# Performance work log

Measured on AMD Instinct MI355X. Metric: run time of the kernel, lower is better.

## Reference

```python
import jax, jax.numpy as jnp
import numpy as np

N_HEAD = 16

def setup_inputs() -> dict:
    key = jax.random.key(0)
    ks = jax.random.split(key, 5)
    d = 1024
    x = jax.random.normal(ks[0], (2, 2048, d), dtype=jnp.float32)
    Wqkv = jax.random.normal(ks[1], (d, 3 * d), dtype=jnp.float32) * (1.0 / np.sqrt(d))
    bqkv = jnp.zeros((3 * d,), dtype=jnp.float32)
    Wproj = jax.random.normal(ks[2], (d, d), dtype=jnp.float32) * (1.0 / np.sqrt(d))
    bproj = jnp.zeros((d,), dtype=jnp.float32)
    return {"x": x, "Wqkv": Wqkv, "bqkv": bqkv, "Wproj": Wproj, "bproj": bproj}


def reference(x, Wqkv, bqkv, Wproj, bproj):
    B, T, C = x.shape
    H = N_HEAD
    Dh = C // H
    qkv = x @ Wqkv + bqkv                      # [B, T, 3C]
    q, k, v = jnp.split(qkv, 3, axis=-1)
    # [B, T, C] -> [B, H, T, Dh]
    q = q.reshape(B, T, H, Dh).transpose(0, 2, 1, 3)
    k = k.reshape(B, T, H, Dh).transpose(0, 2, 1, 3)
    v = v.reshape(B, T, H, Dh).transpose(0, 2, 1, 3)
    scale = 1.0 / np.sqrt(Dh)
    att = jnp.einsum('bhqd,bhkd->bhqk', q, k) * scale
    causal = jnp.tril(jnp.ones((T, T), dtype=bool))
    att = jnp.where(causal[None, None, :, :], att, jnp.float32(-jnp.inf))
    att = jax.nn.softmax(att, axis=-1)
    y = jnp.einsum('bhqk,bhkd->bhqd', att, v)  # [B, H, T, Dh]
    y = y.transpose(0, 2, 1, 3).reshape(B, T, C)
    return y @ Wproj + bproj
```

## Files before the change

kernel.cpp:

```cpp
#include <hip/hip_runtime.h>
#include <math.h>


typedef __attribute__((ext_vector_type(8))) short short8;
typedef __attribute__((ext_vector_type(4))) short short4v;
typedef __attribute__((ext_vector_type(4))) float floatx4;
typedef __attribute__((ext_vector_type(16))) float floatx16;
typedef __attribute__((ext_vector_type(2))) unsigned int uint2v;
typedef __attribute__((ext_vector_type(4))) unsigned int uint4v;

__device__ __forceinline__ unsigned short f2bf(float f) {
  unsigned u = __float_as_uint(f);
  return (unsigned short)((u + 0x7fff + ((u >> 16) & 1)) >> 16);
}

__device__ __forceinline__ unsigned cvtpk(float a, float b) {
  unsigned r;
  asm("v_cvt_pk_bf16_f32 %0, %1, %2" : "=v"(r) : "v"(a), "v"(b));
  return r;
}

__device__ __forceinline__ short8 mk8(unsigned w0, unsigned w1, unsigned w2,
                                      unsigned w3) {
  uint4v v = {w0, w1, w2, w3};
  return __builtin_bit_cast(short8, v);
}

__device__ __forceinline__ void gld16(const unsigned short* g, unsigned short* l) {
  __builtin_amdgcn_global_load_lds(
      (const __attribute__((address_space(1))) unsigned int*)g,
      (__attribute__((address_space(3))) unsigned int*)l, 16, 0, 0);
}

__device__ __forceinline__ void pack_a_body(const float* __restrict__ in,
                                            unsigned short* __restrict__ out,
                                            int K, int m0, int k0,
                                            unsigned short (*lds)[72], int t) {
  {
    int ml = t >> 2, kl = (t & 3) * 16;
    const float4* p = (const float4*)(in + (size_t)(m0 + ml) * K + k0 + kl);
    unsigned short* q = &lds[ml][kl];
#pragma unroll
    for (int c = 0; c < 4; ++c) {
      float4 v = p[c];
      q[c * 4 + 0] = f2bf(v.x);
      q[c * 4 + 1] = f2bf(v.y);
      q[c * 4 + 2] = f2bf(v.z);
      q[c * 4 + 3] = f2bf(v.w);
    }
  }
  __syncthreads();
  int chunk = t >> 3, sub = t & 7;
  int mt = chunk >> 3, kc = chunk & 7;
  unsigned short tmp[16];
#pragma unroll
  for (int j2 = 0; j2 < 2; ++j2)
#pragma unroll
    for (int j = 0; j < 8; ++j)
      tmp[j2 * 8 + j] = lds[mt * 16 + sub * 2 + j2][kc * 8 + j];
  size_t ofs = ((size_t)(m0 >> 4) + mt) * (16 * (size_t)K) +
               ((size_t)(k0 >> 3) + kc) * 128 + sub * 16;
  *(int4*)(out + ofs) = *(int4*)(tmp);
  *(int4*)(out + ofs + 8) = *(int4*)(tmp + 8);
}

__device__ __forceinline__ void pack_bt_body(const float* __restrict__ in,
                                             unsigned short* __restrict__ out,
                                             int K, int N, int n0, int k0,
                                             unsigned short (*lds)[72], int t) {
  {
    int kl = t >> 2, nl = (t & 3) * 16;
    const float4* p = (const float4*)(in + (size_t)(k0 + kl) * N + n0 + nl);
#pragma unroll
    for (int c = 0; c < 4; ++c) {
      float4 v = p[c];
      lds[nl + c * 4 + 0][kl] = f2bf(v.x);
      lds[nl + c * 4 + 1][kl] = f2bf(v.y);
      lds[nl + c * 4 + 2][kl] = f2bf(v.z);
      lds[nl + c * 4 + 3][kl] = f2bf(v.w);
    }
  }
  __syncthreads();
  int chunk = t >> 3, sub = t & 7;
  int nt = chunk >> 3, kc = chunk & 7;
  unsigned short tmp[16];
#pragma unroll
  for (int j2 = 0; j2 < 2; ++j2)
#pragma unroll
    for (int j = 0; j < 8; ++j)
      tmp[j2 * 8 + j] = lds[nt * 16 + sub * 2 + j2][kc * 8 + j];
  size_t ofs = ((size_t)(n0 >> 4) + nt) * (16 * (size_t)K) +
               ((size_t)(k0 >> 3) + kc) * 128 + sub * 16;
  *(int4*)(out + ofs) = *(int4*)(tmp);
  *(int4*)(out + ofs + 8) = *(int4*)(tmp + 8);
}

__global__ __launch_bounds__(256) void pack_all(
    const float* __restrict__ x, const float* __restrict__ Wqkv,
    const float* __restrict__ Wproj, unsigned short* __restrict__ xbf,
    unsigned short* __restrict__ wqkvF, unsigned short* __restrict__ wprojF) {
  __shared__ __align__(16) unsigned short lds[64][72];
  const int b = blockIdx.x, t = threadIdx.x;
  if (b < 1024) {
    pack_a_body(x, xbf, 1024, (b >> 4) * 64, (b & 15) * 64, lds, t);
  } else if (b < 1792) {
    int b2 = b - 1024;
    pack_bt_body(Wqkv, wqkvF, 1024, 3072, (b2 % 48) * 64, (b2 / 48) * 64, lds, t);
  } else {
    int b3 = b - 1792;
    pack_bt_body(Wproj, wprojF, 1024, 1024, (b3 & 15) * 64, (b3 >> 4) * 64, lds, t);
  }
}

template <int MODE>
__global__ __launch_bounds__(256, 3) void gemm_lds(
    const unsigned short* __restrict__ A, const unsigned short* __restrict__ B,
    const float* __restrict__ bias, float* __restrict__ Cout,
    unsigned short* __restrict__ Qb, unsigned short* __restrict__ Kb,
    unsigned short* __restrict__ Vt, int M, int N, int K) {
  const int tid = threadIdx.x;
  const int wave = tid >> 6, lane = tid & 63;
  const int quad = lane >> 4, l15 = lane & 15;
  const int wr = wave >> 1, wc = wave & 1;

  const int nbn = N >> 7;
  const int colsPerX = nbn >> 3;
  const int xcd = (int)(blockIdx.x & 7);
  const int idx = (int)(blockIdx.x >> 3);
  const int bn = xcd * colsPerX + (colsPerX == 1 ? 0 : (idx % colsPerX));
  const int bm = (colsPerX == 1) ? idx : (idx / colsPerX);

  const int mt0 = bm * 8;
  const int nt0 = bn * 8;

  __shared__ __align__(16) unsigned short As[8192];
  __shared__ __align__(16) unsigned short Bs[8192];

  const unsigned short* spA[4];
  const unsigned short* spB[4];
#pragma unroll
  for (int j = 0; j < 4; ++j) {
    int c = wave * 4 + j;
    spA[j] = A + ((size_t)(mt0 + (c >> 1))) * (16 * (size_t)K) +
             (c & 1) * 512 + lane * 8;
    spB[j] = B + ((size_t)(nt0 + (c >> 1))) * (16 * (size_t)K) +
             (c & 1) * 512 + lane * 8;
  }

  floatx4 acc[4][4];
#pragma unroll
  for (int i = 0; i < 4; ++i)
#pragma unroll
    for (int j = 0; j < 4; ++j) acc[i][j] = (floatx4)0.0f;

  const int fofs = quad * 128 + l15 * 8;
  const int nk = K >> 6;

  for (int kk = 0; kk < nk; ++kk) {
#pragma unroll
    for (int j = 0; j < 4; ++j) {
      gld16(spA[j], &As[(wave * 4 + j) * 512]);
      gld16(spB[j], &Bs[(wave * 4 + j) * 512]);
      spA[j] += 1024;
      spB[j] += 1024;
    }
    __syncthreads();

#pragma unroll
    for (int ks = 0; ks < 2; ++ks) {
      short8 fa[4], fb[4];
#pragma unroll
      for (int im = 0; im < 4; ++im)
        fa[im] = *(const short8*)&As[((wr * 4 + im) * 2 + ks) * 512 + fofs];
#pragma unroll
      for (int in = 0; in < 4; ++in)
        fb[in] = *(const short8*)&Bs[((wc * 4 + in) * 2 + ks) * 512 + fofs];
#pragma unroll
      for (int im = 0; im < 4; ++im)
#pragma unroll
        for (int in = 0; in < 4; ++in)
          acc[im][in] = __builtin_amdgcn_mfma_f32_16x16x32_bf16(
              fa[im], fb[in], acc[im][in], 0, 0, 0);
    }
    if (kk + 1 < nk) __syncthreads();
  }

  const int m0w = bm * 128 + wr * 64;
  const int n0w = bn * 128 + wc * 64;

  if (MODE == 0) {
    const float QSCALE = 0.18033688f;
#pragma unroll
    for (int im = 0; im < 4; ++im) {
      int mbase = m0w + im * 16 + quad * 4;
      int bb = mbase >> 11, tb = mbase & 2047;
#pragma unroll
      for (int in = 0; in < 4; ++in) {
        int n = n0w + in * 16 + l15;
        float bv = bias[n];
        int which = n >> 10;
        int h = (n >> 6) & 15;
        int d = n & 63;
        size_t bh_ = (size_t)(bb * 16 + h);
        if (which == 2) {
          size_t base = bh_ * 131072 + (size_t)(d >> 5) * 65536 +
                        (size_t)(tb >> 4) * 512 +
                        (size_t)((d & 31) + 32 * ((tb & 15) >> 3)) * 8 +
                        (tb & 7);
          short4v pk;
#pragma unroll
          for (int r = 0; r < 4; ++r) pk[r] = (short)f2bf(acc[im][in][r] + bv);
          *(short4v*)(Vt + base) = pk;
        } else {
          size_t base = bh_ * 131072 + (size_t)(tb >> 5) * 2048 +
                        (size_t)(d >> 4) * 512 +
                        (size_t)((tb & 31) + 32 * ((d & 15) >> 3)) * 8 +
                        (d & 7);
          if (which == 0) {
#pragma unroll
            for (int r = 0; r < 4; ++r)
              Qb[base + r * 8] = f2bf((acc[im][in][r] + bv) * QSCALE);
          } else {
#pragma unroll
            for (int r = 0; r < 4; ++r)
              Kb[base + r * 8] = f2bf(acc[im][in][r] + bv);
          }
        }
      }
    }
  } else {
#pragma unroll
    for (int im = 0; im < 4; ++im) {
      int mbase = m0w + im * 16 + quad * 4;
#pragma unroll
      for (int in = 0; in < 4; ++in) {
        int n = n0w + in * 16 + l15;
        float bv = bias[n];
#pragma unroll
        for (int r = 0; r < 4; ++r)
          Cout[(size_t)(mbase + r) * N + n] = acc[im][in][r] + bv;
      }
    }
  }
}

__device__ __forceinline__ void pack_swap(const floatx16& s, short8& lo,
                                          short8& hi) {
  unsigned P0 = cvtpk(s[0], s[1]), P1 = cvtpk(s[2], s[3]);
  unsigned P2 = cvtpk(s[4], s[5]), P3 = cvtpk(s[6], s[7]);
  unsigned P4 = cvtpk(s[8], s[9]), P5 = cvtpk(s[10], s[11]);
  unsigned P6 = cvtpk(s[12], s[13]), P7 = cvtpk(s[14], s[15]);
  uint2v a = __builtin_amdgcn_permlane32_swap(P0, P2, false, false);
  uint2v b = __builtin_amdgcn_permlane32_swap(P1, P3, false, false);
  uint2v c = __builtin_amdgcn_permlane32_swap(P4, P6, false, false);
  uint2v d = __builtin_amdgcn_permlane32_swap(P5, P7, false, false);
  lo = mk8(a.x, b.x, a.y, b.y);
  hi = mk8(c.x, d.x, c.y, d.y);
}

__global__ __launch_bounds__(256, 2) void attn_mfma(
    const unsigned short* __restrict__ Q, const unsigned short* __restrict__ K,
    const unsigned short* __restrict__ Vt, unsigned short* __restrict__ Y) {
  const int b = (int)blockIdx.x;
  const int xcd = b & 7, qi = b >> 3;
  const int bh = xcd * 4 + (qi & 3);
  const int m = 15 - (qi >> 2);
  const int wave = threadIdx.x >> 6;
  const int lane = threadIdx.x & 63;
  const int j = m * 4 + wave;
  const int t0 = j * 32;
  const int l31 = lane & 31, h = lane >> 5;

  const unsigned short* Qb = Q + (size_t)bh * 131072;
  const unsigned short* Kb = K + (size_t)bh * 131072;
  const unsigned short* Vb = Vt + (size_t)bh * 131072;
  const int lofs = lane * 8;

  short8 qf[4];
#pragma unroll
  for (int c = 0; c < 4; ++c)
    qf[c] = *(const short8*)(Qb + (size_t)j * 2048 + c * 512 + lofs);

  floatx16 o0 = (floatx16)0.0f, o1 = (floatx16)0.0f;
  float lp[4] = {0.f, 0.f, 0.f, 0.f};

  const int ntiles = (j >> 1) + 1;

  short8 kf[2][4];
#pragma unroll
  for (int c = 0; c < 4; ++c) {
    kf[0][c] = *(const short8*)(Kb + c * 512 + lofs);
    kf[1][c] = *(const short8*)(Kb + 2048 + c * 512 + lofs);
  }

  for (int jt = 0; jt < ntiles; ++jt) {
    short8 vf[2][4];
#pragma unroll
    for (int kc = 0; kc < 4; ++kc) {
      vf[0][kc] = *(const short8*)(Vb + (size_t)(4 * jt + kc) * 512 + lofs);
      vf[1][kc] =
          *(const short8*)(Vb + 65536 + (size_t)(4 * jt + kc) * 512 + lofs);
    }

    floatx16 sa0 = (floatx16)0.0f, sa1 = (floatx16)0.0f;
#pragma unroll
    for (int c = 0; c < 4; ++c) {
      sa0 = __builtin_amdgcn_mfma_f32_32x32x16_bf16(kf[0][c], qf[c], sa0, 0, 0, 0);
      sa1 = __builtin_amdgcn_mfma_f32_32x32x16_bf16(kf[1][c], qf[c], sa1, 0, 0, 0);
    }

    if (jt + 1 < ntiles) {
#pragma unroll
      for (int c = 0; c < 4; ++c) {
        kf[0][c] =
            *(const short8*)(Kb + (size_t)(2 * jt + 2) * 2048 + c * 512 + lofs);
        kf[1][c] =
            *(const short8*)(Kb + (size_t)(2 * jt + 3) * 2048 + c * 512 + lofs);
      }
    }

    if (jt == ntiles - 1) {
#pragma unroll
      for (int r = 0; r < 16; ++r) {
        int row = (r & 3) + 8 * (r >> 2) + 4 * h;
        int key = jt * 64 + row;
        if (key > t0 + l31) sa0[r] = -__builtin_inff();
        if (key + 32 > t0 + l31) sa1[r] = -__builtin_inff();
      }
    }

#pragma unroll
    for (int r = 0; r < 16; ++r) {
      float p0 = exp2f(sa0[r]);
      float p1 = exp2f(sa1[r]);
      sa0[r] = p0;
      sa1[r] = p1;
      lp[r & 3] += p0 + p1;
    }

    short8 pb0, pb1, pb2, pb3;
    pack_swap(sa0, pb0, pb1);
    pack_swap(sa1, pb2, pb3);

    o0 = __builtin_amdgcn_mfma_f32_32x32x16_bf16(vf[0][0], pb0, o0, 0, 0, 0);
    o1 = __builtin_amdgcn_mfma_f32_32x32x16_bf16(vf[1][0], pb0, o1, 0, 0, 0);
    o0 = __builtin_amdgcn_mfma_f32_32x32x16_bf16(vf[0][1], pb1, o0, 0, 0, 0);
    o1 = __builtin_amdgcn_mfma_f32_32x32x16_bf16(vf[1][1], pb1, o1, 0, 0, 0);
    o0 = __builtin_amdgcn_mfma_f32_32x32x16_bf16(vf[0][2], pb2, o0, 0, 0, 0);
    o1 = __builtin_amdgcn_mfma_f32_32x32x16_bf16(vf[1][2], pb2, o1, 0, 0, 0);
    o0 = __builtin_amdgcn_mfma_f32_32x32x16_bf16(vf[0][3], pb3, o0, 0, 0, 0);
    o1 = __builtin_amdgcn_mfma_f32_32x32x16_bf16(vf[1][3], pb3, o1, 0, 0, 0);
  }

  float l_acc = (lp[0] + lp[1]) + (lp[2] + lp[3]);
  l_acc += __shfl_xor(l_acc, 32);
  const float inv = 1.0f / l_acc;

  const int b_ = bh >> 4, hh = bh & 15;
  const int mglob = b_ * 2048 + t0 + l31;
  const size_t mofs = (size_t)(mglob >> 4) * 16384 + (size_t)(mglob & 15) * 8;
#pragma unroll
  for (int db = 0; db < 2; ++db) {
    const floatx16& o = db ? o1 : o0;
#pragma unroll
    for (int g = 0; g < 4; ++g) {
      int d0 = db * 32 + 8 * g + 4 * h;
      int kf0 = hh * 64 + d0;
      size_t ofs = mofs + (size_t)(kf0 >> 3) * 128 + (kf0 & 7);
      short4v pk;
#pragma unroll
      for (int r = 0; r < 4; ++r) pk[r] = (short)f2bf(o[4 * g + r] * inv);
      *(short4v*)(Y + ofs) = pk;
    }
  }
}

extern "C" void kernel_launch(void* const* d_in, const int* in_sizes, int n_in,
                              void* d_out, int out_size, void* d_ws,
                              size_t ws_size, hipStream_t stream) {
  const float* x = (const float*)d_in[0];
  const float* Wqkv = (const float*)d_in[1];
  const float* bqkv = (const float*)d_in[2];
  const float* Wproj = (const float*)d_in[3];
  const float* bproj = (const float*)d_in[4];
  float* out = (float*)d_out;

  const int C = 1024;
  const int M = 4096;

  char* ws = (char*)d_ws;
  unsigned short* qbuf = (unsigned short*)ws;
  unsigned short* kbuf = (unsigned short*)(ws + 8388608);
  unsigned short* vtbuf = (unsigned short*)(ws + 16777216);
  unsigned short* ybuf = (unsigned short*)(ws + 25165824);
  unsigned short* xbf = (unsigned short*)(ws + 33554432);
  unsigned short* wqkvF = (unsigned short*)(ws + 41943040);
  unsigned short* wprojF = (unsigned short*)(ws + 48234496);

  dim3 blk(256);
  pack_all<<<dim3(2048), blk, 0, stream>>>(x, Wqkv, Wproj, xbf, wqkvF, wprojF);
  gemm_lds<0><<<dim3((M / 128) * (3 * C / 128)), blk, 0, stream>>>(
      xbf, wqkvF, bqkv, nullptr, qbuf, kbuf, vtbuf, M, 3 * C, C);
  attn_mfma<<<dim3(512), blk, 0, stream>>>(qbuf, kbuf, vtbuf, ybuf);
  gemm_lds<1><<<dim3((M / 128) * (C / 128)), blk, 0, stream>>>(
      ybuf, wprojF, bproj, out, nullptr, nullptr, nullptr, M, C, C);
}
```

Baseline: 179.5 us.

## Share K/V tiles across waves via double-buffered LDS staging in attention

Each wave in the attention kernel used to fetch its own K and V fragments from global memory, even though all four waves in a block work on the same head. Now the four waves cooperatively stage each K/V tile into a double-buffered shared-memory buffer with global_load_lds, and every wave then reads the fragments from LDS. The goal is to cut redundant global/L2 traffic by sharing each tile across the block and to overlap the next tile's load with compute. The cost is two block barriers per iteration. The loop also now runs to the block-wide maximum tile count, so the lower waves process one extra fully masked tile.

New measurement: 178.7 us. No clear change (-0.4%).

```diff
diff --git a/kernel.cpp b/kernel.cpp
--- a/kernel.cpp
+++ b/kernel.cpp
@@ -30,6 +30,13 @@
   __builtin_amdgcn_global_load_lds(
       (const __attribute__((address_space(1))) unsigned int*)g,
       (__attribute__((address_space(3))) unsigned int*)l, 16, 0, 0);
+}
+
+__device__ __forceinline__ void vmcnt4() {
+  asm volatile("s_waitcnt vmcnt(4)" ::: "memory");
+}
+__device__ __forceinline__ void vmcnt0() {
+  asm volatile("s_waitcnt vmcnt(0)" ::: "memory");
 }
 
 __device__ __forceinline__ void pack_a_body(const float* __restrict__ in,
@@ -270,56 +277,64 @@
   const int j = m * 4 + wave;
   const int t0 = j * 32;
   const int l31 = lane & 31, h = lane >> 5;
+  const int lofs8 = lane * 8;
+
+  __shared__ __align__(16) unsigned short KV[2][8192];
 
   const unsigned short* Qb = Q + (size_t)bh * 131072;
   const unsigned short* Kb = K + (size_t)bh * 131072;
   const unsigned short* Vb = Vt + (size_t)bh * 131072;
-  const int lofs = lane * 8;
+
+  auto stage = [&](int buf, int jtN) {
+    unsigned short* l = &KV[buf][wave * 2048];
+    const unsigned short* g =
+        (wave < 2) ? (Kb + (size_t)jtN * 4096 + wave * 2048)
+                   : (Vb + (size_t)(wave & 1) * 65536 + (size_t)jtN * 2048);
+    g += lofs8;
+#pragma unroll
+    for (int i = 0; i < 4; ++i) gld16(g + i * 512, l + i * 512);
+  };
 
   short8 qf[4];
 #pragma unroll
   for (int c = 0; c < 4; ++c)
-    qf[c] = *(const short8*)(Qb + (size_t)j * 2048 + c * 512 + lofs);
+    qf[c] = *(const short8*)(Qb + (size_t)j * 2048 + c * 512 + lofs8);
 
   floatx16 o0 = (floatx16)0.0f, o1 = (floatx16)0.0f;
   float lp[4] = {0.f, 0.f, 0.f, 0.f};
 
   const int ntiles = (j >> 1) + 1;
-
-  short8 kf[2][4];
-#pragma unroll
-  for (int c = 0; c < 4; ++c) {
-    kf[0][c] = *(const short8*)(Kb + c * 512 + lofs);
-    kf[1][c] = *(const short8*)(Kb + 2048 + c * 512 + lofs);
-  }
-
-  for (int jt = 0; jt < ntiles; ++jt) {
-    short8 vf[2][4];
-#pragma unroll
-    for (int kc = 0; kc < 4; ++kc) {
-      vf[0][kc] = *(const short8*)(Vb + (size_t)(4 * jt + kc) * 512 + lofs);
-      vf[1][kc] =
-          *(const short8*)(Vb + 65536 + (size_t)(4 * jt + kc) * 512 + lofs);
+  const int ntB = 2 * m + 2;
+
+  stage(0, 0);
+  int cur = 0;
+
+  for (int jt = 0; jt < ntB; ++jt) {
+    if (jt + 1 < ntB) {
+      stage(cur ^ 1, jt + 1);
+      vmcnt4();
+    } else {
+      vmcnt0();
+    }
+    __builtin_amdgcn_s_barrier();
+    __builtin_amdgcn_sched_barrier(0);
+
+    const unsigned short* Lb = KV[cur];
+    short8 kf0[4], kf1[4];
+#pragma unroll
+    for (int c = 0; c < 4; ++c) {
+      kf0[c] = *(const short8*)&Lb[c * 512 + lofs8];
+      kf1[c] = *(const short8*)&Lb[2048 + c * 512 + lofs8];
     }
 
     floatx16 sa0 = (floatx16)0.0f, sa1 = (floatx16)0.0f;
 #pragma unroll
     for (int c = 0; c < 4; ++c) {
-      sa0 = __builtin_amdgcn_mfma_f32_32x32x16_bf16(kf[0][c], qf[c], sa0, 0, 0, 0);
-      sa1 = __builtin_amdgcn_mfma_f32_32x32x16_bf16(kf[1][c], qf[c], sa1, 0, 0, 0);
-    }
-
-    if (jt + 1 < ntiles) {
-#pragma unroll
-      for (int c = 0; c < 4; ++c) {
-        kf[0][c] =
-            *(const short8*)(Kb + (size_t)(2 * jt + 2) * 2048 + c * 512 + lofs);
-        kf[1][c] =
-            *(const short8*)(Kb + (size_t)(2 * jt + 3) * 2048 + c * 512 + lofs);
-      }
-    }
-
-    if (jt == ntiles - 1) {
+      sa0 = __builtin_amdgcn_mfma_f32_32x32x16_bf16(kf0[c], qf[c], sa0, 0, 0, 0);
+      sa1 = __builtin_amdgcn_mfma_f32_32x32x16_bf16(kf1[c], qf[c], sa1, 0, 0, 0);
+    }
+
+    if (jt >= ntiles - 1) {
 #pragma unroll
       for (int r = 0; r < 16; ++r) {
         int row = (r & 3) + 8 * (r >> 2) + 4 * h;
@@ -342,14 +357,25 @@
     pack_swap(sa0, pb0, pb1);
     pack_swap(sa1, pb2, pb3);
 
-    o0 = __builtin_amdgcn_mfma_f32_32x32x16_bf16(vf[0][0], pb0, o0, 0, 0, 0);
-    o1 = __builtin_amdgcn_mfma_f32_32x32x16_bf16(vf[1][0], pb0, o1, 0, 0, 0);
-    o0 = __builtin_amdgcn_mfma_f32_32x32x16_bf16(vf[0][1], pb1, o0, 0, 0, 0);
-    o1 = __builtin_amdgcn_mfma_f32_32x32x16_bf16(vf[1][1], pb1, o1, 0, 0, 0);
-    o0 = __builtin_amdgcn_mfma_f32_32x32x16_bf16(vf[0][2], pb2, o0, 0, 0, 0);
-    o1 = __builtin_amdgcn_mfma_f32_32x32x16_bf16(vf[1][2], pb2, o1, 0, 0, 0);
-    o0 = __builtin_amdgcn_mfma_f32_32x32x16_bf16(vf[0][3], pb3, o0, 0, 0, 0);
-    o1 = __builtin_amdgcn_mfma_f32_32x32x16_bf16(vf[1][3], pb3, o1, 0, 0, 0);
+    short8 vf0[4], vf1[4];
+#pragma unroll
+    for (int kc = 0; kc < 4; ++kc) {
+      vf0[kc] = *(const short8*)&Lb[4096 + kc * 512 + lofs8];
+      vf1[kc] = *(const short8*)&Lb[6144 + kc * 512 + lofs8];
+    }
+
+    o0 = __builtin_amdgcn_mfma_f32_32x32x16_bf16(vf0[0], pb0, o0, 0, 0, 0);
+    o1 = __builtin_amdgcn_mfma_f32_32x32x16_bf16(vf1[0], pb0, o1, 0, 0, 0);
+    o0 = __builtin_amdgcn_mfma_f32_32x32x16_bf16(vf0[1], pb1, o0, 0, 0, 0);
+    o1 = __builtin_amdgcn_mfma_f32_32x32x16_bf16(vf1[1], pb1, o1, 0, 0, 0);
+    o0 = __builtin_amdgcn_mfma_f32_32x32x16_bf16(vf0[2], pb2, o0, 0, 0, 0);
+    o1 = __builtin_amdgcn_mfma_f32_32x32x16_bf16(vf1[2], pb2, o1, 0, 0, 0);
+    o0 = __builtin_amdgcn_mfma_f32_32x32x16_bf16(vf0[3], pb3, o0, 0, 0, 0);
+    o1 = __builtin_amdgcn_mfma_f32_32x32x16_bf16(vf1[3], pb3, o1, 0, 0, 0);
+
+    __builtin_amdgcn_sched_barrier(0);
+    __builtin_amdgcn_s_barrier();
+    cur ^= 1;
   }
 
   float l_acc = (lp[0] + lp[1]) + (lp[2] + lp[3]);
```
